# Performance work log

Hardware: AMD Instinct MI355X
Metric: run time of the kernel (lower is better)

Reference implementation:

```python
import jax, jax.numpy as jnp
import numpy as np

N_NODES = 50000
N_EDGES = 800000
F = 64
EPS = 1e-5


def batchnorm(x, gamma, beta):
    # training-mode BatchNorm1d: batch mean, biased variance
    mu = jnp.mean(x, axis=0)
    var = jnp.mean((x - mu) ** 2, axis=0)
    return gamma * (x - mu) * jax.lax.rsqrt(var + EPS) + beta


def setup_inputs() -> dict:
    key = jax.random.key(0)
    ks = jax.random.split(key, 10)
    s = 1.0 / np.sqrt(3 * F)
    return {
        "node_feats": jax.random.normal(ks[0], (N_NODES, F), jnp.float32),
        "edge_feats": jax.random.normal(ks[1], (N_EDGES, F), jnp.float32),
        "src": jax.random.randint(ks[2], (N_EDGES,), 0, N_NODES, jnp.int32),
        "dst": jax.random.randint(ks[3], (N_EDGES,), 0, N_NODES, jnp.int32),
        "W_mlpt": jax.random.uniform(ks[4], (3 * F, F), jnp.float32, -s, s),
        "b_mlpt": jnp.zeros((F,), jnp.float32),
        "g_mlpt": jnp.ones((F,), jnp.float32),
        "be_mlpt": jnp.zeros((F,), jnp.float32),
        "W_gate": jax.random.uniform(ks[5], (3 * F, F), jnp.float32, -s, s),
        "b_gate": jnp.zeros((F,), jnp.float32),
        "g_gate": jnp.ones((F,), jnp.float32),
        "be_gate": jnp.zeros((F,), jnp.float32),
        "g_node": jnp.ones((F,), jnp.float32),
        "be_node": jnp.zeros((F,), jnp.float32),
    }


def reference(node_feats, edge_feats, src, dst,
              W_mlpt, b_mlpt, g_mlpt, be_mlpt,
              W_gate, b_gate, g_gate, be_gate,
              g_node, be_node):
    # edge-wise gather + concat: [E, 3F]
    h_cat = jnp.concatenate(
        [node_feats[src], node_feats[dst], edge_feats], axis=1)
    # two small MLPs: Linear + BN + activation (dropout p=0)
    h_mlpt = jax.nn.sigmoid(batchnorm(h_cat @ W_mlpt + b_mlpt, g_mlpt, be_mlpt))
    h_gate = jax.nn.softplus(batchnorm(h_cat @ W_gate + b_gate, g_gate, be_gate))
    h_upd = h_mlpt * h_gate  # [E, F]
    # scatter-sum messages onto destination nodes
    agg = jax.ops.segment_sum(h_upd, dst, num_segments=N_NODES)  # [N, F]
    node_out = jax.nn.sigmoid(batchnorm(agg, g_node, be_node) + node_feats)
    return (node_out, edge_feats)
```

## Files before the change

### kernel.cpp

```cpp
#include <hip/hip_runtime.h>

#define E_TOT   800000
#define NN      50000
#define FF      64

typedef __attribute__((ext_vector_type(8))) short  short8;
typedef __attribute__((ext_vector_type(4))) float  f32x4;

__device__ __forceinline__ unsigned short f2bf(float f) {
  union { float f; unsigned int u; } v; v.f = f;
  unsigned int r = v.u + 0x7fffu + ((v.u >> 16) & 1u);
  return (unsigned short)(r >> 16);
}

__device__ __forceinline__ unsigned int pkbf(float a, float b) {
  unsigned int r;
  asm("v_cvt_pk_bf16_f32 %0, %1, %2" : "=v"(r) : "v"(a), "v"(b));
  return r;
}

__device__ __forceinline__ float sigmoidf_(float x) {
  return 1.f / (1.f + __expf(-x));
}

__global__ void pack_w(const float* __restrict__ Wm, const float* __restrict__ Wg,
                       unsigned short* __restrict__ Wp) {
  int t = blockIdx.x * 256 + threadIdx.x;
  if (t >= 3072) return;
  int lane = t & 63;
  int kk   = (t >> 6) % 6;
  int mnt  = t / 384;
  const float* W = (mnt >> 2) ? Wg : Wm;
  int nt  = mnt & 3;
  int col = nt * 16 + (lane & 15);
  int kb  = kk * 32 + (lane >> 4) * 8;
  #pragma unroll
  for (int j = 0; j < 8; ++j)
    Wp[t * 8 + j] = f2bf(W[(kb + j) * 64 + col]);
}

__global__ __launch_bounds__(256)
void edge_gemm(const float* __restrict__ nodef, const float* __restrict__ edgef,
               const int* __restrict__ src, const int* __restrict__ dst,
               const unsigned short* __restrict__ Wp,
               float* __restrict__ stats,
               uint4* __restrict__ Yw)
{
  __shared__ unsigned short sh[64 * 200];

  const int tid = threadIdx.x;
  const int e0  = blockIdx.x * 64;
  const int row = tid >> 2;
  const int cq  = tid & 3;

  const int s = src[e0 + row], d = dst[e0 + row];
  const float* ps = nodef + (size_t)s * 64 + cq * 4;
  const float* pd = nodef + (size_t)d * 64 + cq * 4;
  const float* pe = edgef + (size_t)(e0 + row) * 64 + cq * 4;
  unsigned short* sp = &sh[row * 200 + cq * 4];

  #pragma unroll
  for (int it = 0; it < 4; ++it) {
    float4 v0 = *(const float4*)(ps + it * 16);
    float4 v1 = *(const float4*)(pd + it * 16);
    float4 v2 = *(const float4*)(pe + it * 16);
    uint2 w0 = make_uint2(pkbf(v0.x, v0.y), pkbf(v0.z, v0.w));
    uint2 w1 = make_uint2(pkbf(v1.x, v1.y), pkbf(v1.z, v1.w));
    uint2 w2 = make_uint2(pkbf(v2.x, v2.y), pkbf(v2.z, v2.w));
    *(uint2*)(sp +   0 + it * 16) = w0;
    *(uint2*)(sp +  64 + it * 16) = w1;
    *(uint2*)(sp + 128 + it * 16) = w2;
  }
  __syncthreads();

  const int w = tid >> 6, lane = tid & 63;
  f32x4 acc[8] = {};
  const unsigned short* abase = &sh[(w * 16 + (lane & 15)) * 200 + (lane >> 4) * 8];
  const short8* wp = (const short8*)Wp;

  #pragma unroll
  for (int kk = 0; kk < 6; ++kk) {
    short8 a = *(const short8*)(abase + kk * 32);
    #pragma unroll
    for (int nt = 0; nt < 8; ++nt) {
      short8 b = wp[(nt * 6 + kk) * 64 + lane];
      acc[nt] = __builtin_amdgcn_mfma_f32_16x16x32_bf16(a, b, acc[nt], 0, 0, 0);
    }
  }

  uint4* yb = Yw + (((size_t)blockIdx.x * 4 + w) * 4) * 64 + lane;
  #pragma unroll
  for (int ntp = 0; ntp < 4; ++ntp) {
    uint4 q;
    q.x = pkbf(acc[2 * ntp][0],     acc[2 * ntp][1]);
    q.y = pkbf(acc[2 * ntp][2],     acc[2 * ntp][3]);
    q.z = pkbf(acc[2 * ntp + 1][0], acc[2 * ntp + 1][1]);
    q.w = pkbf(acc[2 * ntp + 1][2], acc[2 * ntp + 1][3]);
    yb[ntp * 64] = q;
  }

  __shared__ float red[4 * 256];
  #pragma unroll
  for (int nt = 0; nt < 8; ++nt) {
    float sv = acc[nt][0] + acc[nt][1] + acc[nt][2] + acc[nt][3];
    float qv = acc[nt][0] * acc[nt][0] + acc[nt][1] * acc[nt][1] +
               acc[nt][2] * acc[nt][2] + acc[nt][3] * acc[nt][3];
    sv += __shfl_xor(sv, 16); sv += __shfl_xor(sv, 32);
    qv += __shfl_xor(qv, 16); qv += __shfl_xor(qv, 32);
    if ((lane >> 4) == 0) {
      red[w * 256 + nt * 16 + lane]       = sv;
      red[w * 256 + 128 + nt * 16 + lane] = qv;
    }
  }
  __syncthreads();
  float v = red[tid] + red[256 + tid] + red[512 + tid] + red[768 + tid];
  atomicAdd(&stats[(blockIdx.x & 63) * 256 + tid], v);
}

__global__ __launch_bounds__(256)
void edge_apply(const uint4* __restrict__ Yw, const int* __restrict__ dst,
                const float* __restrict__ coef,
                float* __restrict__ agg)
{
  const int tid = threadIdx.x;
  const int w = tid >> 6, lane = tid & 63;
  const int e0 = blockIdx.x * 64;
  const int r0 = w * 16 + ((lane >> 4) << 2);
  const int4 dn = *(const int4*)&dst[e0 + r0];
  const int colb = lane & 15;

  const uint4* yb = Yw + (((size_t)blockIdx.x * 4 + w) * 4) * 64 + lane;
  uint4 qm0 = yb[0], qm1 = yb[64], qg0 = yb[128], qg1 = yb[192];
  const unsigned int um[8] = {qm0.x, qm0.y, qm0.z, qm0.w, qm1.x, qm1.y, qm1.z, qm1.w};
  const unsigned int ug[8] = {qg0.x, qg0.y, qg0.z, qg0.w, qg1.x, qg1.y, qg1.z, qg1.w};

  const int dr[4] = {dn.x, dn.y, dn.z, dn.w};

  #pragma unroll
  for (int ntm = 0; ntm < 4; ++ntm) {
    const int col = ntm * 16 + colb;
    const float am = coef[col],      cm = coef[128 + col];
    const float ag = coef[64 + col], cg = coef[192 + col];
    #pragma unroll
    for (int p = 0; p < 2; ++p) {
      unsigned int m = um[ntm * 2 + p], g = ug[ntm * 2 + p];
      #pragma unroll
      for (int h = 0; h < 2; ++h) {
        float mv = __uint_as_float(h ? (m & 0xffff0000u) : (m << 16));
        float gv = __uint_as_float(h ? (g & 0xffff0000u) : (g << 16));
        float ym = fmaf(mv, am, cm);
        float yg = fmaf(gv, ag, cg);
        float sig = sigmoidf_(ym);
        float sp  = (yg > 20.f) ? yg : __logf(1.f + __expf(yg));
        int r = 2 * p + h;
        atomicAdd(&agg[(size_t)dr[r] * 64 + col], sig * sp);
      }
    }
  }
}

__global__ void finalize_edge(const float* __restrict__ stats,
                              const float* __restrict__ g_m, const float* __restrict__ be_m,
                              const float* __restrict__ g_g, const float* __restrict__ be_g,
                              float* __restrict__ coef) {
  int c = threadIdx.x;
  float s = 0.f, q = 0.f;
  for (int sl = 0; sl < 64; ++sl) { s += stats[sl * 256 + c]; q += stats[sl * 256 + 128 + c]; }
  float mu  = s * (1.f / E_TOT);
  float var = fmaxf(q * (1.f / E_TOT) - mu * mu, 0.f);
  float g   = (c < 64) ? g_m[c]  : g_g[c - 64];
  float be  = (c < 64) ? be_m[c] : be_g[c - 64];
  float a   = g * rsqrtf(var + 1e-5f);
  coef[c]       = a;
  coef[128 + c] = be - mu * a;
}

__global__ void node_stats(const float* __restrict__ agg, float* __restrict__ nstats) {
  __shared__ float rs[256], rq[256];
  int tid = threadIdx.x;
  int col = tid & 63;
  float s = 0.f, q = 0.f;
  for (int r = blockIdx.x * 4 + (tid >> 6); r < NN; r += gridDim.x * 4) {
    float v = agg[r * 64 + col];
    s += v; q += v * v;
  }
  rs[tid] = s; rq[tid] = q;
  __syncthreads();
  if (tid < 64) {
    s = rs[tid] + rs[tid + 64] + rs[tid + 128] + rs[tid + 192];
    q = rq[tid] + rq[tid + 64] + rq[tid + 128] + rq[tid + 192];
    int slot = blockIdx.x & 31;
    atomicAdd(&nstats[slot * 128 + col], s);
    atomicAdd(&nstats[slot * 128 + 64 + col], q);
  }
}

__global__ void finalize_node(const float* __restrict__ nstats,
                              const float* __restrict__ g_n, const float* __restrict__ be_n,
                              float* __restrict__ coefn) {
  int c = threadIdx.x;
  float s = 0.f, q = 0.f;
  for (int sl = 0; sl < 32; ++sl) { s += nstats[sl * 128 + c]; q += nstats[sl * 128 + 64 + c]; }
  float mu  = s * (1.f / NN);
  float var = fmaxf(q * (1.f / NN) - mu * mu, 0.f);
  float a   = g_n[c] * rsqrtf(var + 1e-5f);
  coefn[c]      = a;
  coefn[64 + c] = be_n[c] - mu * a;
}

__global__ void node_out_k(float* __restrict__ out, const float* __restrict__ nodef,
                           const float* __restrict__ coefn) {
  int i  = blockIdx.x * 256 + threadIdx.x;
  int cb = (i & 15) * 4;
  float4 a  = ((float4*)out)[i];
  float4 nf = ((const float4*)nodef)[i];
  float4 r;
  r.x = sigmoidf_(coefn[cb + 0] * a.x + coefn[64 + cb + 0] + nf.x);
  r.y = sigmoidf_(coefn[cb + 1] * a.y + coefn[64 + cb + 1] + nf.y);
  r.z = sigmoidf_(coefn[cb + 2] * a.z + coefn[64 + cb + 2] + nf.z);
  r.w = sigmoidf_(coefn[cb + 3] * a.w + coefn[64 + cb + 3] + nf.w);
  ((float4*)out)[i] = r;
}

extern "C" void kernel_launch(void* const* d_in, const int* in_sizes, int n_in,
                              void* d_out, int out_size, void* d_ws, size_t ws_size,
                              hipStream_t stream) {
  const float* nodef = (const float*)d_in[0];
  const float* edgef = (const float*)d_in[1];
  const int*   src   = (const int*)d_in[2];
  const int*   dst   = (const int*)d_in[3];
  const float* W_m   = (const float*)d_in[4];
  const float* g_m   = (const float*)d_in[6];
  const float* be_m  = (const float*)d_in[7];
  const float* W_g   = (const float*)d_in[8];
  const float* g_g   = (const float*)d_in[10];
  const float* be_g  = (const float*)d_in[11];
  const float* g_n   = (const float*)d_in[12];
  const float* be_n  = (const float*)d_in[13];

  float* out = (float*)d_out;
  float* agg = out;
  uint4* Yw  = (uint4*)(out + (size_t)NN * FF);

  char*  ws  = (char*)d_ws;
  float*          stats  = (float*)ws;
  float*          coef   = (float*)(ws + 65536);
  float*          nstats = (float*)(ws + 66560);
  float*          coefn  = (float*)(ws + 82944);
  unsigned short* Wp     = (unsigned short*)(ws + 83456);

  hipMemsetAsync(agg, 0, (size_t)NN * FF * sizeof(float), stream);
  hipMemsetAsync(d_ws, 0, 83456, stream);

  pack_w<<<12, 256, 0, stream>>>(W_m, W_g, Wp);
  edge_gemm<<<E_TOT / 64, 256, 0, stream>>>(nodef, edgef, src, dst, Wp, stats, Yw);
  finalize_edge<<<1, 128, 0, stream>>>(stats, g_m, be_m, g_g, be_g, coef);
  edge_apply<<<E_TOT / 64, 256, 0, stream>>>(Yw, dst, coef, agg);
  hipMemcpyAsync(out + (size_t)NN * FF, edgef, (size_t)E_TOT * FF * sizeof(float),
                 hipMemcpyDeviceToDevice, stream);
  node_stats<<<512, 256, 0, stream>>>(agg, nstats);
  finalize_node<<<1, 64, 0, stream>>>(nstats, g_n, be_n, coefn);
  node_out_k<<<NN * FF / 4 / 256, 256, 0, stream>>>(agg, nodef, coefn);
}
```

Before: 444.3 us.

## Replace atomic scatter with CSR-by-destination segmented sum and fuse edge copy

Drops the per-element atomicAdd scatter of edge messages. It builds a destination-sorted CSR index: edge_gemm counts degrees, a single-block scan turns the counts into offsets, and fill_k writes edge ids per slot. node_sum then uses one wavefront per node to gather bf16 pre-activations, apply BN, sigmoid and softplus, and write the aggregate without atomics. When the workspace is large enough, Y is stored row-major in the workspace and the edge_feats output copy is folded into edge_gemm. The costs are extra kernels, including a serial single-block scan, and a random gather of Y rows, and the order of summation depends on the atomic fill order.

```diff
diff --git a/kernel.cpp b/kernel.cpp
--- a/kernel.cpp
+++ b/kernel.cpp
@@ -39,43 +39,51 @@
     Wp[t * 8 + j] = f2bf(W[(kb + j) * 64 + col]);
 }
 
-__global__ __launch_bounds__(256)
+__global__ __launch_bounds__(256, 6)
 void edge_gemm(const float* __restrict__ nodef, const float* __restrict__ edgef,
                const int* __restrict__ src, const int* __restrict__ dst,
                const unsigned short* __restrict__ Wp,
-               float* __restrict__ stats,
-               uint4* __restrict__ Yw)
+               float* __restrict__ stats, int* __restrict__ counts,
+               unsigned short* __restrict__ Y, float* __restrict__ outE,
+               int write_copy)
 {
-  __shared__ unsigned short sh[64 * 200];
+  __shared__ unsigned short buf[64 * 200];
+  float* red = (float*)(buf + 64 * 136);
 
   const int tid = threadIdx.x;
   const int e0  = blockIdx.x * 64;
   const int row = tid >> 2;
   const int cq  = tid & 3;
 
+  if (tid < 64) atomicAdd(&counts[dst[e0 + tid]], 1);
+
   const int s = src[e0 + row], d = dst[e0 + row];
   const float* ps = nodef + (size_t)s * 64 + cq * 4;
   const float* pd = nodef + (size_t)d * 64 + cq * 4;
   const float* pe = edgef + (size_t)(e0 + row) * 64 + cq * 4;
-  unsigned short* sp = &sh[row * 200 + cq * 4];
-
+  unsigned short* sp = &buf[row * 200 + cq * 4];
+
+  float4 ev[4];
   #pragma unroll
   for (int it = 0; it < 4; ++it) {
     float4 v0 = *(const float4*)(ps + it * 16);
     float4 v1 = *(const float4*)(pd + it * 16);
     float4 v2 = *(const float4*)(pe + it * 16);
-    uint2 w0 = make_uint2(pkbf(v0.x, v0.y), pkbf(v0.z, v0.w));
-    uint2 w1 = make_uint2(pkbf(v1.x, v1.y), pkbf(v1.z, v1.w));
-    uint2 w2 = make_uint2(pkbf(v2.x, v2.y), pkbf(v2.z, v2.w));
-    *(uint2*)(sp +   0 + it * 16) = w0;
-    *(uint2*)(sp +  64 + it * 16) = w1;
-    *(uint2*)(sp + 128 + it * 16) = w2;
+    ev[it] = v2;
+    *(uint2*)(sp +   0 + it * 16) = make_uint2(pkbf(v0.x, v0.y), pkbf(v0.z, v0.w));
+    *(uint2*)(sp +  64 + it * 16) = make_uint2(pkbf(v1.x, v1.y), pkbf(v1.z, v1.w));
+    *(uint2*)(sp + 128 + it * 16) = make_uint2(pkbf(v2.x, v2.y), pkbf(v2.z, v2.w));
+  }
+  if (write_copy) {
+    float4* op = (float4*)(outE + (size_t)(e0 + row) * 64 + cq * 4);
+    #pragma unroll
+    for (int it = 0; it < 4; ++it) op[it * 4] = ev[it];
   }
   __syncthreads();
 
   const int w = tid >> 6, lane = tid & 63;
   f32x4 acc[8] = {};
-  const unsigned short* abase = &sh[(w * 16 + (lane & 15)) * 200 + (lane >> 4) * 8];
+  const unsigned short* abase = &buf[(w * 16 + (lane & 15)) * 200 + (lane >> 4) * 8];
   const short8* wp = (const short8*)Wp;
 
   #pragma unroll
@@ -88,18 +96,19 @@
     }
   }
 
-  uint4* yb = Yw + (((size_t)blockIdx.x * 4 + w) * 4) * 64 + lane;
-  #pragma unroll
-  for (int ntp = 0; ntp < 4; ++ntp) {
-    uint4 q;
-    q.x = pkbf(acc[2 * ntp][0],     acc[2 * ntp][1]);
-    q.y = pkbf(acc[2 * ntp][2],     acc[2 * ntp][3]);
-    q.z = pkbf(acc[2 * ntp + 1][0], acc[2 * ntp + 1][1]);
-    q.w = pkbf(acc[2 * ntp + 1][2], acc[2 * ntp + 1][3]);
-    yb[ntp * 64] = q;
-  }
-
-  __shared__ float red[4 * 256];
+  __syncthreads();
+
+  const int colb = lane & 15, rq = lane >> 4;
+  #pragma unroll
+  for (int nt = 0; nt < 8; ++nt) {
+    int col = nt * 16 + colb;
+    #pragma unroll
+    for (int r = 0; r < 4; ++r) {
+      int rw = w * 16 + rq * 4 + r;
+      buf[rw * 136 + col] = (unsigned short)pkbf(acc[nt][r], acc[nt][r]);
+    }
+  }
+
   #pragma unroll
   for (int nt = 0; nt < 8; ++nt) {
     float sv = acc[nt][0] + acc[nt][1] + acc[nt][2] + acc[nt][3];
@@ -113,50 +122,17 @@
     }
   }
   __syncthreads();
+
+  #pragma unroll
+  for (int k2 = 0; k2 < 4; ++k2) {
+    int k    = tid + k2 * 256;
+    int rw   = k >> 4, part = k & 15;
+    uint4 v  = *(const uint4*)&buf[rw * 136 + part * 8];
+    *(uint4*)&Y[(size_t)(e0 + rw) * 128 + part * 8] = v;
+  }
+
   float v = red[tid] + red[256 + tid] + red[512 + tid] + red[768 + tid];
   atomicAdd(&stats[(blockIdx.x & 63) * 256 + tid], v);
-}
-
-__global__ __launch_bounds__(256)
-void edge_apply(const uint4* __restrict__ Yw, const int* __restrict__ dst,
-                const float* __restrict__ coef,
-                float* __restrict__ agg)
-{
-  const int tid = threadIdx.x;
-  const int w = tid >> 6, lane = tid & 63;
-  const int e0 = blockIdx.x * 64;
-  const int r0 = w * 16 + ((lane >> 4) << 2);
-  const int4 dn = *(const int4*)&dst[e0 + r0];
-  const int colb = lane & 15;
-
-  const uint4* yb = Yw + (((size_t)blockIdx.x * 4 + w) * 4) * 64 + lane;
-  uint4 qm0 = yb[0], qm1 = yb[64], qg0 = yb[128], qg1 = yb[192];
-  const unsigned int um[8] = {qm0.x, qm0.y, qm0.z, qm0.w, qm1.x, qm1.y, qm1.z, qm1.w};
-  const unsigned int ug[8] = {qg0.x, qg0.y, qg0.z, qg0.w, qg1.x, qg1.y, qg1.z, qg1.w};
-
-  const int dr[4] = {dn.x, dn.y, dn.z, dn.w};
-
-  #pragma unroll
-  for (int ntm = 0; ntm < 4; ++ntm) {
-    const int col = ntm * 16 + colb;
-    const float am = coef[col],      cm = coef[128 + col];
-    const float ag = coef[64 + col], cg = coef[192 + col];
-    #pragma unroll
-    for (int p = 0; p < 2; ++p) {
-      unsigned int m = um[ntm * 2 + p], g = ug[ntm * 2 + p];
-      #pragma unroll
-      for (int h = 0; h < 2; ++h) {
-        float mv = __uint_as_float(h ? (m & 0xffff0000u) : (m << 16));
-        float gv = __uint_as_float(h ? (g & 0xffff0000u) : (g << 16));
-        float ym = fmaf(mv, am, cm);
-        float yg = fmaf(gv, ag, cg);
-        float sig = sigmoidf_(ym);
-        float sp  = (yg > 20.f) ? yg : __logf(1.f + __expf(yg));
-        int r = 2 * p + h;
-        atomicAdd(&agg[(size_t)dr[r] * 64 + col], sig * sp);
-      }
-    }
-  }
 }
 
 __global__ void finalize_edge(const float* __restrict__ stats,
@@ -173,6 +149,108 @@
   float a   = g * rsqrtf(var + 1e-5f);
   coef[c]       = a;
   coef[128 + c] = be - mu * a;
+}
+
+__global__ __launch_bounds__(1024)
+void scan_k(const int* __restrict__ counts, int* __restrict__ offs, int* __restrict__ cursor) {
+  __shared__ int wsum[16];
+  const int t = threadIdx.x;
+  const int CH = 49;
+  int lo = t * CH, hi = min(lo + CH, NN);
+  if (lo > NN) lo = NN;
+  int s = 0;
+  for (int i = lo; i < hi; ++i) s += counts[i];
+  int lane = t & 63, w = t >> 6;
+  int v = s;
+  #pragma unroll
+  for (int dlt = 1; dlt < 64; dlt <<= 1) {
+    int u = __shfl_up(v, dlt);
+    if (lane >= dlt) v += u;
+  }
+  if (lane == 63) wsum[w] = v;
+  __syncthreads();
+  if (t == 0) {
+    int a = 0;
+    for (int i = 0; i < 16; ++i) { int c = wsum[i]; wsum[i] = a; a += c; }
+  }
+  __syncthreads();
+  int run = v - s + wsum[w];
+  for (int i = lo; i < hi; ++i) {
+    int c = counts[i];
+    offs[i] = run; cursor[i] = run;
+    run += c;
+  }
+}
+
+__global__ void fill_k(const int* __restrict__ dst, int* __restrict__ cursor,
+                       int* __restrict__ eid) {
+  int e = blockIdx.x * 256 + threadIdx.x;
+  if (e < E_TOT) {
+    int p = atomicAdd(&cursor[dst[e]], 1);
+    eid[p] = e;
+  }
+}
+
+__global__ __launch_bounds__(256)
+void node_sum(const unsigned int* __restrict__ Yu, const int* __restrict__ offs,
+              const int* __restrict__ counts, const int* __restrict__ eid,
+              const float* __restrict__ coef, float* __restrict__ agg)
+{
+  const int tid = threadIdx.x;
+  const int lane = tid & 63, w = tid >> 6;
+  const int gw = blockIdx.x * 4 + w;
+  const int l = lane & 31;
+  const bool hi = lane >= 32;
+
+  const float A0 = hi ? coef[64 + 2 * l]  : coef[2 * l];
+  const float A1 = hi ? coef[65 + 2 * l]  : coef[2 * l + 1];
+  const float C0 = hi ? coef[192 + 2 * l] : coef[128 + 2 * l];
+  const float C1 = hi ? coef[193 + 2 * l] : coef[128 + 2 * l + 1];
+
+  for (int n = gw; n < NN; n += 8192) {
+    const int st = offs[n], deg = counts[n];
+    float a0 = 0.f, a1 = 0.f;
+
+    for (int base = 0; base < deg; base += 64) {
+      int m = min(64, deg - base);
+      int ev = (lane < m) ? eid[st + base + lane] : 0;
+
+      int j = 0;
+      for (; j + 4 <= m; j += 4) {
+        int ea = __shfl(ev, j), eb = __shfl(ev, j + 1);
+        int ec = __shfl(ev, j + 2), ed = __shfl(ev, j + 3);
+        unsigned int ya = Yu[(size_t)ea * 64 + lane];
+        unsigned int yb = Yu[(size_t)eb * 64 + lane];
+        unsigned int yc = Yu[(size_t)ec * 64 + lane];
+        unsigned int yd = Yu[(size_t)ed * 64 + lane];
+        #pragma unroll
+        for (int q = 0; q < 4; ++q) {
+          unsigned int y = (q == 0) ? ya : (q == 1) ? yb : (q == 2) ? yc : yd;
+          float f0 = __uint_as_float(y << 16);
+          float f1 = __uint_as_float(y & 0xffff0000u);
+          float v0 = fmaf(f0, A0, C0), v1 = fmaf(f1, A1, C1);
+          float x0 = __expf(hi ? v0 : -v0), x1 = __expf(hi ? v1 : -v1);
+          float r0 = hi ? ((v0 > 20.f) ? v0 : __logf(1.f + x0)) : 1.f / (1.f + x0);
+          float r1 = hi ? ((v1 > 20.f) ? v1 : __logf(1.f + x1)) : 1.f / (1.f + x1);
+          float p0 = __shfl_xor(r0, 32), p1 = __shfl_xor(r1, 32);
+          a0 += r0 * p0; a1 += r1 * p1;
+        }
+      }
+      for (; j < m; ++j) {
+        int ea = __shfl(ev, j);
+        unsigned int y = Yu[(size_t)ea * 64 + lane];
+        float f0 = __uint_as_float(y << 16);
+        float f1 = __uint_as_float(y & 0xffff0000u);
+        float v0 = fmaf(f0, A0, C0), v1 = fmaf(f1, A1, C1);
+        float x0 = __expf(hi ? v0 : -v0), x1 = __expf(hi ? v1 : -v1);
+        float r0 = hi ? ((v0 > 20.f) ? v0 : __logf(1.f + x0)) : 1.f / (1.f + x0);
+        float r1 = hi ? ((v1 > 20.f) ? v1 : __logf(1.f + x1)) : 1.f / (1.f + x1);
+        float p0 = __shfl_xor(r0, 32), p1 = __shfl_xor(r1, 32);
+        a0 += r0 * p0; a1 += r1 * p1;
+      }
+    }
+    if (!hi) *(float2*)&agg[(size_t)n * 64 + 2 * l] = make_float2(a0, a1);
+  }
 }
 
 __global__ void node_stats(const float* __restrict__ agg, float* __restrict__ nstats) {
@@ -238,26 +316,40 @@
   const float* g_n   = (const float*)d_in[12];
   const float* be_n  = (const float*)d_in[13];
 
-  float* out = (float*)d_out;
-  float* agg = out;
-  uint4* Yw  = (uint4*)(out + (size_t)NN * FF);
-
-  char*  ws  = (char*)d_ws;
-  float*          stats  = (float*)ws;
-  float*          coef   = (float*)(ws + 65536);
-  float*          nstats = (float*)(ws + 66560);
-  float*          coefn  = (float*)(ws + 82944);
-  unsigned short* Wp     = (unsigned short*)(ws + 83456);
-
-  hipMemsetAsync(agg, 0, (size_t)NN * FF * sizeof(float), stream);
-  hipMemsetAsync(d_ws, 0, 83456, stream);
+  float* out  = (float*)d_out;
+  float* agg  = out;
+  float* outE = out + (size_t)NN * FF;
+
+  char* ws = (char*)d_ws;
+  int*   counts = (int*)(ws + 0x000000);
+  int*   offs   = (int*)(ws + 0x040000);
+  int*   cursor = (int*)(ws + 0x080000);
+  int*   eid    = (int*)(ws + 0x0C0000);
+  float* stats  = (float*)(ws + 0x400000);
+  float* coef   = (float*)(ws + 0x410000);
+  float* nstats = (float*)(ws + 0x411000);
+  float* coefn  = (float*)(ws + 0x415000);
+  unsigned short* Wp = (unsigned short*)(ws + 0x416000);
+
+  const size_t y_bytes = (size_t)E_TOT * 128 * 2;
+  const int y_in_ws = (ws_size >= (size_t)(8 << 20) + y_bytes);
+  unsigned short* Y = y_in_ws ? (unsigned short*)(ws + (8 << 20))
+                              : (unsigned short*)outE;
+
+  hipMemsetAsync(counts, 0, NN * sizeof(int), stream);
+  hipMemsetAsync(stats, 0, 0x15200, stream);
 
   pack_w<<<12, 256, 0, stream>>>(W_m, W_g, Wp);
-  edge_gemm<<<E_TOT / 64, 256, 0, stream>>>(nodef, edgef, src, dst, Wp, stats, Yw);
+  edge_gemm<<<E_TOT / 64, 256, 0, stream>>>(nodef, edgef, src, dst, Wp,
+                                            stats, counts, Y, outE, y_in_ws);
   finalize_edge<<<1, 128, 0, stream>>>(stats, g_m, be_m, g_g, be_g, coef);
-  edge_apply<<<E_TOT / 64, 256, 0, stream>>>(Yw, dst, coef, agg);
-  hipMemcpyAsync(out + (size_t)NN * FF, edgef, (size_t)E_TOT * FF * sizeof(float),
-                 hipMemcpyDeviceToDevice, stream);
+  scan_k<<<1, 1024, 0, stream>>>(counts, offs, cursor);
+  fill_k<<<(E_TOT + 255) / 256, 256, 0, stream>>>(dst, cursor, eid);
+  node_sum<<<2048, 256, 0, stream>>>((const unsigned int*)Y, offs, counts, eid, coef, agg);
+  if (!y_in_ws) {
+    hipMemcpyAsync(outE, edgef, (size_t)E_TOT * FF * sizeof(float),
+                   hipMemcpyDeviceToDevice, stream);
+  }
   node_stats<<<512, 256, 0, stream>>>(agg, nstats);
   finalize_node<<<1, 64, 0, stream>>>(nstats, g_n, be_n, coefn);
   node_out_k<<<NN * FF / 4 / 256, 256, 0, stream>>>(agg, nodef, coefn);
```

Result: slower. 511.8 us (+15.2%).

## Scatter messages with packed bf16 atomics and fuse edge copy into GEMM

Applied to the files above, without the earlier changes.

The scatter-sum now accumulates into a bf16 buffer in workspace using packed bf16 atomic adds, pairing adjacent columns via a lane shuffle. This halves the number of atomics and the aggregation traffic. When the workspace is large enough, the intermediate Y buffer moves to workspace and the edge_feats passthrough copy is written directly from edge_gemm, removing the separate memcpy. Accumulating sums in bf16 loses precision, since each node receives about 16 messages, which risks tolerance failures.

```diff
diff --git a/kernel.cpp b/kernel.cpp
--- a/kernel.cpp
+++ b/kernel.cpp
@@ -18,6 +18,13 @@
   asm("v_cvt_pk_bf16_f32 %0, %1, %2" : "=v"(r) : "v"(a), "v"(b));
   return r;
 }
+
+__device__ __forceinline__ void atomic_pk_bf16(unsigned short* p, unsigned int v) {
+  asm volatile("global_atomic_pk_add_bf16 %0, %1, off" :: "v"(p), "v"(v) : "memory");
+}
+
+__device__ __forceinline__ float bflo(unsigned int u) { return __uint_as_float(u << 16); }
+__device__ __forceinline__ float bfhi(unsigned int u) { return __uint_as_float(u & 0xffff0000u); }
 
 __device__ __forceinline__ float sigmoidf_(float x) {
   return 1.f / (1.f + __expf(-x));
@@ -39,14 +46,16 @@
     Wp[t * 8 + j] = f2bf(W[(kb + j) * 64 + col]);
 }
 
-__global__ __launch_bounds__(256)
+__global__ __launch_bounds__(256, 5)
 void edge_gemm(const float* __restrict__ nodef, const float* __restrict__ edgef,
                const int* __restrict__ src, const int* __restrict__ dst,
                const unsigned short* __restrict__ Wp,
                float* __restrict__ stats,
-               uint4* __restrict__ Yw)
+               uint4* __restrict__ Yw,
+               float* __restrict__ outE, int write_copy)
 {
   __shared__ unsigned short sh[64 * 200];
+  __shared__ float red[4 * 256];
 
   const int tid = threadIdx.x;
   const int e0  = blockIdx.x * 64;
@@ -59,17 +68,21 @@
   const float* pe = edgef + (size_t)(e0 + row) * 64 + cq * 4;
   unsigned short* sp = &sh[row * 200 + cq * 4];
 
+  float4 ev[4];
   #pragma unroll
   for (int it = 0; it < 4; ++it) {
     float4 v0 = *(const float4*)(ps + it * 16);
     float4 v1 = *(const float4*)(pd + it * 16);
     float4 v2 = *(const float4*)(pe + it * 16);
-    uint2 w0 = make_uint2(pkbf(v0.x, v0.y), pkbf(v0.z, v0.w));
-    uint2 w1 = make_uint2(pkbf(v1.x, v1.y), pkbf(v1.z, v1.w));
-    uint2 w2 = make_uint2(pkbf(v2.x, v2.y), pkbf(v2.z, v2.w));
-    *(uint2*)(sp +   0 + it * 16) = w0;
-    *(uint2*)(sp +  64 + it * 16) = w1;
-    *(uint2*)(sp + 128 + it * 16) = w2;
+    ev[it] = v2;
+    *(uint2*)(sp +   0 + it * 16) = make_uint2(pkbf(v0.x, v0.y), pkbf(v0.z, v0.w));
+    *(uint2*)(sp +  64 + it * 16) = make_uint2(pkbf(v1.x, v1.y), pkbf(v1.z, v1.w));
+    *(uint2*)(sp + 128 + it * 16) = make_uint2(pkbf(v2.x, v2.y), pkbf(v2.z, v2.w));
+  }
+  if (write_copy) {
+    float4* op = (float4*)(outE + (size_t)(e0 + row) * 64 + cq * 4);
+    #pragma unroll
+    for (int it = 0; it < 4; ++it) op[it * 4] = ev[it];
   }
   __syncthreads();
 
@@ -99,7 +112,6 @@
     yb[ntp * 64] = q;
   }
 
-  __shared__ float red[4 * 256];
   #pragma unroll
   for (int nt = 0; nt < 8; ++nt) {
     float sv = acc[nt][0] + acc[nt][1] + acc[nt][2] + acc[nt][3];
@@ -115,48 +127,6 @@
   __syncthreads();
   float v = red[tid] + red[256 + tid] + red[512 + tid] + red[768 + tid];
   atomicAdd(&stats[(blockIdx.x & 63) * 256 + tid], v);
-}
-
-__global__ __launch_bounds__(256)
-void edge_apply(const uint4* __restrict__ Yw, const int* __restrict__ dst,
-                const float* __restrict__ coef,
-                float* __restrict__ agg)
-{
-  const int tid = threadIdx.x;
-  const int w = tid >> 6, lane = tid & 63;
-  const int e0 = blockIdx.x * 64;
-  const int r0 = w * 16 + ((lane >> 4) << 2);
-  const int4 dn = *(const int4*)&dst[e0 + r0];
-  const int colb = lane & 15;
-
-  const uint4* yb = Yw + (((size_t)blockIdx.x * 4 + w) * 4) * 64 + lane;
-  uint4 qm0 = yb[0], qm1 = yb[64], qg0 = yb[128], qg1 = yb[192];
-  const unsigned int um[8] = {qm0.x, qm0.y, qm0.z, qm0.w, qm1.x, qm1.y, qm1.z, qm1.w};
-  const unsigned int ug[8] = {qg0.x, qg0.y, qg0.z, qg0.w, qg1.x, qg1.y, qg1.z, qg1.w};
-
-  const int dr[4] = {dn.x, dn.y, dn.z, dn.w};
-
-  #pragma unroll
-  for (int ntm = 0; ntm < 4; ++ntm) {
-    const int col = ntm * 16 + colb;
-    const float am = coef[col],      cm = coef[128 + col];
-    const float ag = coef[64 + col], cg = coef[192 + col];
-    #pragma unroll
-    for (int p = 0; p < 2; ++p) {
-      unsigned int m = um[ntm * 2 + p], g = ug[ntm * 2 + p];
-      #pragma unroll
-      for (int h = 0; h < 2; ++h) {
-        float mv = __uint_as_float(h ? (m & 0xffff0000u) : (m << 16));
-        float gv = __uint_as_float(h ? (g & 0xffff0000u) : (g << 16));
-        float ym = fmaf(mv, am, cm);
-        float yg = fmaf(gv, ag, cg);
-        float sig = sigmoidf_(ym);
-        float sp  = (yg > 20.f) ? yg : __logf(1.f + __expf(yg));
-        int r = 2 * p + h;
-        atomicAdd(&agg[(size_t)dr[r] * 64 + col], sig * sp);
-      }
-    }
-  }
 }
 
 __global__ void finalize_edge(const float* __restrict__ stats,
@@ -175,23 +145,83 @@
   coef[128 + c] = be - mu * a;
 }
 
-__global__ void node_stats(const float* __restrict__ agg, float* __restrict__ nstats) {
-  __shared__ float rs[256], rq[256];
+__global__ __launch_bounds__(256)
+void edge_apply(const uint4* __restrict__ Yw, const int* __restrict__ dst,
+                const float* __restrict__ coef,
+                unsigned short* __restrict__ aggb)
+{
+  const int tid = threadIdx.x;
+  const int w = tid >> 6, lane = tid & 63;
+  const int e0 = blockIdx.x * 64;
+  const int r0 = w * 16 + ((lane >> 4) << 2);
+  const int4 dn = *(const int4*)&dst[e0 + r0];
+  const int colb = lane & 15;
+  const int par  = colb & 1;
+
+  const uint4* yb = Yw + (((size_t)blockIdx.x * 4 + w) * 4) * 64 + lane;
+  uint4 qm0 = yb[0], qm1 = yb[64], qg0 = yb[128], qg1 = yb[192];
+  const unsigned int um[8] = {qm0.x, qm0.y, qm0.z, qm0.w, qm1.x, qm1.y, qm1.z, qm1.w};
+  const unsigned int ug[8] = {qg0.x, qg0.y, qg0.z, qg0.w, qg1.x, qg1.y, qg1.z, qg1.w};
+  const int dr[4] = {dn.x, dn.y, dn.z, dn.w};
+
+  #pragma unroll
+  for (int ntm = 0; ntm < 4; ++ntm) {
+    const int col = ntm * 16 + colb;
+    const float am = coef[col],      cm = coef[128 + col];
+    const float ag = coef[64 + col], cg = coef[192 + col];
+    float hv[4];
+    #pragma unroll
+    for (int p = 0; p < 2; ++p) {
+      unsigned int m = um[ntm * 2 + p], g = ug[ntm * 2 + p];
+      #pragma unroll
+      for (int h = 0; h < 2; ++h) {
+        float mv = h ? bfhi(m) : bflo(m);
+        float gv = h ? bfhi(g) : bflo(g);
+        float ym = fmaf(mv, am, cm);
+        float yg = fmaf(gv, ag, cg);
+        float sig = sigmoidf_(ym);
+        float sp  = (yg > 20.f) ? yg : __logf(1.f + __expf(yg));
+        hv[2 * p + h] = sig * sp;
+      }
+    }
+    float pv[4];
+    #pragma unroll
+    for (int r = 0; r < 4; ++r) pv[r] = __shfl_xor(hv[r], 1);
+    const int colp = ntm * 16 + (colb & ~1);
+    #pragma unroll
+    for (int rr = 0; rr < 2; ++rr) {
+      int r = par * 2 + rr;
+      float lo = par ? pv[r] : hv[r];
+      float hi = par ? hv[r] : pv[r];
+      atomic_pk_bf16(&aggb[(size_t)dr[r] * 64 + colp], pkbf(lo, hi));
+    }
+  }
+}
+
+__global__ void node_stats(const unsigned int* __restrict__ aggu, float* __restrict__ nstats) {
+  __shared__ float rs0[256], rq0[256], rs1[256], rq1[256];
   int tid = threadIdx.x;
-  int col = tid & 63;
-  float s = 0.f, q = 0.f;
-  for (int r = blockIdx.x * 4 + (tid >> 6); r < NN; r += gridDim.x * 4) {
-    float v = agg[r * 64 + col];
-    s += v; q += v * v;
-  }
-  rs[tid] = s; rq[tid] = q;
+  int cp = tid & 31;
+  float s0 = 0.f, q0 = 0.f, s1 = 0.f, q1 = 0.f;
+  for (int r = blockIdx.x * 8 + (tid >> 5); r < NN; r += gridDim.x * 8) {
+    unsigned int u = aggu[r * 32 + cp];
+    float v0 = bflo(u), v1 = bfhi(u);
+    s0 += v0; q0 += v0 * v0; s1 += v1; q1 += v1 * v1;
+  }
+  rs0[tid] = s0; rq0[tid] = q0; rs1[tid] = s1; rq1[tid] = q1;
   __syncthreads();
-  if (tid < 64) {
-    s = rs[tid] + rs[tid + 64] + rs[tid + 128] + rs[tid + 192];
-    q = rq[tid] + rq[tid + 64] + rq[tid + 128] + rq[tid + 192];
+  if (tid < 32) {
+    s0 = 0.f; q0 = 0.f; s1 = 0.f; q1 = 0.f;
+    #pragma unroll
+    for (int k = 0; k < 8; ++k) {
+      s0 += rs0[tid + 32 * k]; q0 += rq0[tid + 32 * k];
+      s1 += rs1[tid + 32 * k]; q1 += rq1[tid + 32 * k];
+    }
     int slot = blockIdx.x & 31;
-    atomicAdd(&nstats[slot * 128 + col], s);
-    atomicAdd(&nstats[slot * 128 + 64 + col], q);
+    atomicAdd(&nstats[slot * 128 + 2 * tid],      s0);
+    atomicAdd(&nstats[slot * 128 + 2 * tid + 1],  s1);
+    atomicAdd(&nstats[slot * 128 + 64 + 2 * tid],     q0);
+    atomicAdd(&nstats[slot * 128 + 64 + 2 * tid + 1], q1);
   }
 }
 
@@ -208,17 +238,17 @@
   coefn[64 + c] = be_n[c] - mu * a;
 }
 
-__global__ void node_out_k(float* __restrict__ out, const float* __restrict__ nodef,
-                           const float* __restrict__ coefn) {
+__global__ void node_out_k(float* __restrict__ out, const unsigned int* __restrict__ aggu,
+                           const float* __restrict__ nodef, const float* __restrict__ coefn) {
   int i  = blockIdx.x * 256 + threadIdx.x;
   int cb = (i & 15) * 4;
-  float4 a  = ((float4*)out)[i];
+  uint2  u  = ((const uint2*)aggu)[i];
   float4 nf = ((const float4*)nodef)[i];
   float4 r;
-  r.x = sigmoidf_(coefn[cb + 0] * a.x + coefn[64 + cb + 0] + nf.x);
-  r.y = sigmoidf_(coefn[cb + 1] * a.y + coefn[64 + cb + 1] + nf.y);
-  r.z = sigmoidf_(coefn[cb + 2] * a.z + coefn[64 + cb + 2] + nf.z);
-  r.w = sigmoidf_(coefn[cb + 3] * a.w + coefn[64 + cb + 3] + nf.w);
+  r.x = sigmoidf_(coefn[cb + 0] * bflo(u.x) + coefn[64 + cb + 0] + nf.x);
+  r.y = sigmoidf_(coefn[cb + 1] * bfhi(u.x) + coefn[64 + cb + 1] + nf.y);
+  r.z = sigmoidf_(coefn[cb + 2] * bflo(u.y) + coefn[64 + cb + 2] + nf.z);
+  r.w = sigmoidf_(coefn[cb + 3] * bfhi(u.y) + coefn[64 + cb + 3] + nf.w);
   ((float4*)out)[i] = r;
 }
 
@@ -238,27 +268,35 @@
   const float* g_n   = (const float*)d_in[12];
   const float* be_n  = (const float*)d_in[13];
 
-  float* out = (float*)d_out;
-  float* agg = out;
-  uint4* Yw  = (uint4*)(out + (size_t)NN * FF);
-
-  char*  ws  = (char*)d_ws;
-  float*          stats  = (float*)ws;
-  float*          coef   = (float*)(ws + 65536);
-  float*          nstats = (float*)(ws + 66560);
-  float*          coefn  = (float*)(ws + 82944);
-  unsigned short* Wp     = (unsigned short*)(ws + 83456);
-
-  hipMemsetAsync(agg, 0, (size_t)NN * FF * sizeof(float), stream);
-  hipMemsetAsync(d_ws, 0, 83456, stream);
+  float* out  = (float*)d_out;
+  float* outE = out + (size_t)NN * FF;
+
+  char* ws = (char*)d_ws;
+  unsigned short* aggb = (unsigned short*)ws;
+  float* stats  = (float*)(ws + 0x640000);
+  float* coef   = (float*)(ws + 0x650000);
+  float* nstats = (float*)(ws + 0x651000);
+  float* coefn  = (float*)(ws + 0x655000);
+  unsigned short* Wp = (unsigned short*)(ws + 0x656000);
+
+  const size_t y_bytes = (size_t)E_TOT * 128 * 2;
+  const int y_in_ws = (ws_size >= (size_t)0x700000 + y_bytes);
+  uint4* Yw = y_in_ws ? (uint4*)(ws + 0x700000) : (uint4*)outE;
+
+  hipMemsetAsync(aggb, 0, (size_t)NN * FF * 2, stream);
+  hipMemsetAsync(stats, 0, 0x15200, stream);
 
   pack_w<<<12, 256, 0, stream>>>(W_m, W_g, Wp);
-  edge_gemm<<<E_TOT / 64, 256, 0, stream>>>(nodef, edgef, src, dst, Wp, stats, Yw);
+  edge_gemm<<<E_TOT / 64, 256, 0, stream>>>(nodef, edgef, src, dst, Wp,
+                                            stats, Yw, outE, y_in_ws);
   finalize_edge<<<1, 128, 0, stream>>>(stats, g_m, be_m, g_g, be_g, coef);
-  edge_apply<<<E_TOT / 64, 256, 0, stream>>>(Yw, dst, coef, agg);
-  hipMemcpyAsync(out + (size_t)NN * FF, edgef, (size_t)E_TOT * FF * sizeof(float),
-                 hipMemcpyDeviceToDevice, stream);
-  node_stats<<<512, 256, 0, stream>>>(agg, nstats);
+  edge_apply<<<E_TOT / 64, 256, 0, stream>>>(Yw, dst, coef, aggb);
+  if (!y_in_ws) {
+    hipMemcpyAsync(outE, edgef, (size_t)E_TOT * FF * sizeof(float),
+                   hipMemcpyDeviceToDevice, stream);
+  }
+  node_stats<<<512, 256, 0, stream>>>((const unsigned int*)aggb, nstats);
   finalize_node<<<1, 64, 0, stream>>>(nstats, g_n, be_n, coefn);
-  node_out_k<<<NN * FF / 4 / 256, 256, 0, stream>>>(agg, nodef, coefn);
-}
+  node_out_k<<<NN * FF / 4 / 256, 256, 0, stream>>>(out, (const unsigned int*)aggb,
+                                                    nodef, coefn);
+}
```

Result: faster. 431.4 us (-2.9%).
